# Kernel optimization log

Hardware: AMD Instinct MI355X
Metric: run time of the kernel (lower is better)

## Reference

```python
import jax, jax.numpy as jnp
import numpy as np

B, N, E, D, R = 32, 2048, 8192, 512, 8
V_SENSE = 25000
V_GLOBAL = 50000  # last_idx_globals - last_idx_senses


def setup_inputs() -> dict:
    key = jax.random.key(0)
    ks = jax.random.split(key, 12)
    x = jax.random.normal(ks[0], (B, N, D), dtype=jnp.float32)
    edge_index = jax.random.randint(ks[1], (B, 2, E), 0, N)
    edge_type = jax.random.randint(ks[2], (B, E), 0, R)
    s = 0.02
    basis = jax.random.normal(ks[3], (R, D, D), dtype=jnp.float32) * s   # num_bases = R
    comp = jax.random.normal(ks[4], (R, R), dtype=jnp.float32) * s      # [num_relations, num_bases]
    root = jax.random.normal(ks[5], (D, D), dtype=jnp.float32) * s
    bias_conv = jnp.zeros((D,), dtype=jnp.float32)
    w_global = jax.random.normal(ks[6], (V_GLOBAL, D), dtype=jnp.float32) * s
    b_global = jnp.zeros((V_GLOBAL,), dtype=jnp.float32)
    w_sense = jax.random.normal(ks[7], (V_SENSE, D), dtype=jnp.float32) * s
    b_sense = jnp.zeros((V_SENSE,), dtype=jnp.float32)
    return {"x": x, "edge_index": edge_index, "edge_type": edge_type,
            "basis": basis, "comp": comp, "root": root, "bias_conv": bias_conv,
            "w_global": w_global, "b_global": b_global,
            "w_sense": w_sense, "b_sense": b_sense}


def reference(x, edge_index, edge_type, basis, comp, root, bias_conv,
              w_global, b_global, w_sense, b_sense):
    # Basis decomposition: per-relation weight W_r = sum_b comp[r,b] * basis[b]
    W = jnp.einsum('rb,bio->rio', comp, basis)  # [R, D, D]

    def conv_one(xg, ei, et):
        # RGCNConv with mean aggregation per relation + root transform + bias
        src, dst = ei[0], ei[1]
        x_src = xg[src]                              # [E, D] gather
        out = xg @ root + bias_conv                  # [N, D]
        for r in range(R):                           # fixed small relation loop
            mask = (et == r).astype(xg.dtype)        # [E]
            msg = (x_src @ W[r]) * mask[:, None]     # [E, D]
            s = jax.ops.segment_sum(msg, dst, num_segments=N)              # [N, D]
            cnt = jax.ops.segment_sum(mask, dst, num_segments=N)           # [N]
            out = out + s / jnp.maximum(cnt, 1.0)[:, None]                 # mean aggr
        return out

    h = jax.vmap(conv_one)(x, edge_index, edge_type)  # [B, N, D]
    h = jax.nn.relu(h)
    h0 = h[:, 0]                                      # current node per sample [B, D]
    logits_global = h0 @ w_global.T + b_global        # [B, V_GLOBAL]
    logits_sense = h0 @ w_sense.T + b_sense           # [B, V_SENSE]
    return (jax.nn.log_softmax(logits_global, axis=-1),
            jax.nn.log_softmax(logits_sense, axis=-1))
```

## Files before the change

### kernel.cpp

```cpp
#include <hip/hip_runtime.h>
#include <hip/hip_bf16.h>

#define BATCH 32
#define NNODE 2048
#define NEDGE 8192
#define DIM   512
#define NREL  8
#define VG    50000
#define VS    25000
#define ZI    4608
#define NCH   36
#define GB3   391
#define SB3   196
#define PG    25
#define PS    13

typedef __attribute__((ext_vector_type(4))) float f32x4;
typedef __attribute__((ext_vector_type(8))) short s16x8;

__global__ __launch_bounds__(512) void k_conv(const float* __restrict__ x,
                                              const int* __restrict__ ei,
                                              const int* __restrict__ et,
                                              const float* __restrict__ comp,
                                              float* __restrict__ z) {
    int g = blockIdx.x;
    int t = threadIdx.x;
    int wv = t >> 6, lane = t & 63;
    __shared__ int elds[8 * 128];
    __shared__ int wcnt[8];
    const int* srcp = ei + (size_t)(g * 2 + 0) * NEDGE;
    const int* dstp = ei + (size_t)(g * 2 + 1) * NEDGE;

    int run = 0;
    for (int it = 0; it < 16; it++) {
        int e = wv * 1024 + it * 64 + lane;
        bool m = (dstp[e] == 0);
        unsigned long long mask = __ballot(m);
        int rank = __popcll(mask & ((1ull << lane) - 1ull));
        if (m && (run + rank) < 128) elds[wv * 128 + run + rank] = e;
        run += (int)__popcll(mask);
    }
    if (lane == 0) wcnt[wv] = (run > 128) ? 128 : run;
    __syncthreads();

    int d = t;
    float s0=0,s1=0,s2=0,s3=0,s4=0,s5=0,s6=0,s7=0;
    int   c0=0,c1=0,c2=0,c3=0,c4=0,c5=0,c6=0,c7=0;
    for (int w = 0; w < 8; w++) {
        int cw = wcnt[w];
        for (int i = 0; i < cw; i++) {
            int e = elds[w * 128 + i];
            int r = et[(size_t)g * NEDGE + e];
            int sn = srcp[e];
            float val = x[((size_t)g * NNODE + sn) * DIM + d];
            if (r == 0) { s0 += val; c0++; }
            if (r == 1) { s1 += val; c1++; }
            if (r == 2) { s2 += val; c2++; }
            if (r == 3) { s3 += val; c3++; }
            if (r == 4) { s4 += val; c4++; }
            if (r == 5) { s5 += val; c5++; }
            if (r == 6) { s6 += val; c6++; }
            if (r == 7) { s7 += val; c7++; }
        }
    }
    float sv[8] = {s0,s1,s2,s3,s4,s5,s6,s7};
    float inv[8];
    int   cv[8] = {c0,c1,c2,c3,c4,c5,c6,c7};
    #pragma unroll
    for (int r = 0; r < 8; r++) inv[r] = 1.0f / fmaxf((float)cv[r], 1.0f);

    z[(size_t)g * ZI + d] = x[((size_t)g * NNODE + 0) * DIM + d];
    #pragma unroll
    for (int b = 0; b < 8; b++) {
        float y = 0.f;
        #pragma unroll
        for (int r = 0; r < 8; r++) y += comp[r * 8 + b] * inv[r] * sv[r];
        z[(size_t)g * ZI + 512 + b * 512 + d] = y;
    }
}

__global__ __launch_bounds__(512) void k_gemm_part(const float* __restrict__ z,
                                                   const float* __restrict__ root,
                                                   const float* __restrict__ basis,
                                                   float* __restrict__ part2) {
    int bx = blockIdx.x;
    int dt = bx & 3;
    int cc = bx >> 2;
    int t = threadIdx.x;
    int dl = t & 127, gq = t >> 7;
    __shared__ float ztT[128][33];
    #pragma unroll
    for (int rep = 0; rep < 8; rep++) {
        int flat = rep * 512 + t;
        int g = flat >> 7, i = flat & 127;
        ztT[i][g] = z[(size_t)g * ZI + cc * 128 + i];
    }
    __syncthreads();
    const float* M = (cc < 4) ? (root + (size_t)(cc * 128) * 512)
                              : (basis + (size_t)((cc - 4) * 128) * 512);
    float acc[8] = {0,0,0,0,0,0,0,0};
    for (int i = 0; i < 128; i++) {
        float m = M[(size_t)i * 512 + dt * 128 + dl];
        #pragma unroll
        for (int j = 0; j < 8; j++) acc[j] += ztT[i][gq * 8 + j] * m;
    }
    #pragma unroll
    for (int j = 0; j < 8; j++) {
        int g = gq * 8 + j;
        part2[((size_t)cc * 32 + g) * 512 + dt * 128 + dl] = acc[j];
    }
}

__device__ __forceinline__ unsigned bf16rne(float f) {
    unsigned u = __float_as_uint(f);
    return (u + 0x7FFFu + ((u >> 16) & 1u)) >> 16;
}

__global__ __launch_bounds__(256) void k_h0(const float* __restrict__ part2,
                                            const float* __restrict__ bias_conv,
                                            unsigned* __restrict__ h0t) {
    int g = blockIdx.x;
    int p = threadIdx.x;
    int d0 = 2 * p;
    float v0 = bias_conv[d0], v1 = bias_conv[d0 + 1];
    for (int cc = 0; cc < NCH; cc++) {
        const float* pp = part2 + ((size_t)cc * 32 + g) * 512 + d0;
        v0 += pp[0];
        v1 += pp[1];
    }
    v0 = fmaxf(v0, 0.f);
    v1 = fmaxf(v1, 0.f);
    h0t[g * 256 + p] = bf16rne(v0) | (bf16rne(v1) << 16);
}

__device__ __forceinline__ void gload_lds16(const float* gsrc, float* ldst) {
    __builtin_amdgcn_global_load_lds(
        (const __attribute__((address_space(1))) void*)gsrc,
        (__attribute__((address_space(3))) void*)ldst,
        16, 0, 0);
}

__device__ __forceinline__ short f2bf(float f) {
    __hip_bfloat16 h = __float2bfloat16(f);
    return *reinterpret_cast<short*>(&h);
}

__global__ __launch_bounds__(256) void k_logits3(const unsigned* __restrict__ h0t,
                                                 const float* __restrict__ wg,
                                                 const float* __restrict__ bg,
                                                 const float* __restrict__ wsn,
                                                 const float* __restrict__ bsv,
                                                 float* __restrict__ out) {
    __shared__ __align__(16) unsigned char hlds[32768];
    __shared__ __align__(16) unsigned char wlds[2][16384];

    int t = threadIdx.x;
    int bx = blockIdx.x;
    int wv = t >> 6, l = t & 63;

    const float* w; const float* bias; float* ob; int V; int v0;
    if (bx < GB3) { w = wg;  bias = bg;  ob = out;                      V = VG; v0 = bx * 128; }
    else          { w = wsn; bias = bsv; ob = out + (size_t)BATCH * VG; V = VS; v0 = (bx - GB3) * 128; }
    int Vm1 = V - 1;

    #pragma unroll
    for (int rep = 0; rep < 8; rep++) {
        int idx = rep * 256 + t;
        int g = idx >> 6, q = idx & 63;
        uint4 val = *(const uint4*)&h0t[idx * 4];
        *(uint4*)&hlds[g * 1024 + ((q << 4) ^ ((g & 7) << 4))] = val;
    }

    #pragma unroll
    for (int i = 0; i < 4; i++) {
        int o = i * 256 + t;
        int row = o >> 3, g16 = o & 7;
        int vr = v0 + row; if (vr > Vm1) vr = Vm1;
        const float* src = w + (size_t)vr * 512
                         + ((((g16 << 4) ^ ((row & 3) << 5))) >> 2);
        gload_lds16(src, (float*)&wlds[0][o * 16]);
    }
    asm volatile("s_waitcnt vmcnt(0)" ::: "memory");
    __syncthreads();

    f32x4 acc[2][2];
    #pragma unroll
    for (int a = 0; a < 2; a++)
        #pragma unroll
        for (int b = 0; b < 2; b++) acc[a][b] = (f32x4){0.f, 0.f, 0.f, 0.f};

    int g32 = l >> 4;
    int gl  = l & 15;
    int cur = 0;

    for (int kc = 0; kc < 16; kc++) {
        if (kc < 15) {
            #pragma unroll
            for (int i = 0; i < 4; i++) {
                int o = i * 256 + t;
                int row = o >> 3, g16 = o & 7;
                int vr = v0 + row; if (vr > Vm1) vr = Vm1;
                const float* src = w + (size_t)vr * 512 + (kc + 1) * 32
                                 + ((((g16 << 4) ^ ((row & 3) << 5))) >> 2);
                gload_lds16(src, (float*)&wlds[cur ^ 1][o * 16]);
            }
        }

        int abase = (kc * 64 + g32 * 16) ^ ((gl & 7) << 4);
        s16x8 a0 = *(const s16x8*)&hlds[gl * 1024 + abase];
        s16x8 a1 = *(const s16x8*)&hlds[(gl + 16) * 1024 + abase];

        #pragma unroll
        for (int ntl = 0; ntl < 2; ntl++) {
            int rloc = (wv * 2 + ntl) * 16 + gl;
            int boff = rloc * 128 + ((g32 * 32) ^ ((rloc & 3) << 5));
            float4 blo = *(const float4*)&wlds[cur][boff];
            float4 bhi = *(const float4*)&wlds[cur][boff + 16];
            s16x8 bf;
            bf[0] = f2bf(blo.x); bf[1] = f2bf(blo.y);
            bf[2] = f2bf(blo.z); bf[3] = f2bf(blo.w);
            bf[4] = f2bf(bhi.x); bf[5] = f2bf(bhi.y);
            bf[6] = f2bf(bhi.z); bf[7] = f2bf(bhi.w);
            acc[ntl][0] = __builtin_amdgcn_mfma_f32_16x16x32_bf16(a0, bf, acc[ntl][0], 0, 0, 0);
            acc[ntl][1] = __builtin_amdgcn_mfma_f32_16x16x32_bf16(a1, bf, acc[ntl][1], 0, 0, 0);
        }

        asm volatile("s_waitcnt vmcnt(0)" ::: "memory");
        __syncthreads();
        cur ^= 1;
    }

    int lrowb = (l >> 4) * 4;
    #pragma unroll
    for (int ntl = 0; ntl < 2; ntl++) {
        int vv = v0 + (wv * 2 + ntl) * 16 + gl;
        if (vv < V) {
            float bia = bias[vv];
            #pragma unroll
            for (int mt = 0; mt < 2; mt++) {
                #pragma unroll
                for (int j = 0; j < 4; j++) {
                    int g = mt * 16 + lrowb + j;
                    ob[(size_t)g * V + vv] = acc[ntl][mt][j] + bia;
                }
            }
        }
    }
}

__global__ __launch_bounds__(256) void k_lse_part(const float* __restrict__ out,
                                                  float* __restrict__ part) {
    int bx = blockIdx.x;
    int V, ci, pidx;
    const float* row;
    if (bx < 32 * PG) {
        int g = bx / PG; ci = bx % PG; V = VG;
        row = out + (size_t)g * VG;
        pidx = g * PG + ci;
    } else {
        int b2 = bx - 32 * PG;
        int g = b2 / PS; ci = b2 % PS; V = VS;
        row = out + (size_t)BATCH * VG + (size_t)g * VS;
        pidx = 32 * PG + g * PS + ci;
    }
    int t = threadIdx.x;
    float p = 0.f;
    int base = ci * 2048 + t * 8;
    #pragma unroll
    for (int jj = 0; jj < 8; jj++) {
        int idx = base + jj;
        if (idx < V) p += expf(row[idx]);
    }
    #pragma unroll
    for (int s = 1; s < 64; s <<= 1) p += __shfl_xor(p, s);
    __shared__ float wsum[4];
    if ((t & 63) == 0) wsum[t >> 6] = p;
    __syncthreads();
    if (t == 0) part[pidx] = wsum[0] + wsum[1] + wsum[2] + wsum[3];
}

__global__ __launch_bounds__(64) void k_lse_final(const float* __restrict__ part,
                                                  float* __restrict__ lse) {
    int t = threadIdx.x;
    int head = t >> 5, g = t & 31;
    float s = 0.f;
    if (head == 0) { for (int c = 0; c < PG; c++) s += part[g * PG + c]; }
    else           { for (int c = 0; c < PS; c++) s += part[32 * PG + g * PS + c]; }
    lse[t] = logf(s);
}

__global__ __launch_bounds__(256) void k_sub(float* __restrict__ out,
                                             const float* __restrict__ lse) {
    unsigned i4 = blockIdx.x * 256u + threadIdx.x;
    if (i4 >= 600000u) return;
    unsigned idx = i4 * 4u;
    float l;
    if (idx < 1600000u) l = lse[idx / 50000u];
    else                l = lse[32u + (idx - 1600000u) / 25000u];
    float4 v = *(float4*)(out + idx);
    v.x -= l; v.y -= l; v.z -= l; v.w -= l;
    *(float4*)(out + idx) = v;
}

extern "C" void kernel_launch(void* const* d_in, const int* in_sizes, int n_in,
                              void* d_out, int out_size, void* d_ws, size_t ws_size,
                              hipStream_t stream) {
    const float* x        = (const float*)d_in[0];
    const int*   ei       = (const int*)  d_in[1];
    const int*   et       = (const int*)  d_in[2];
    const float* basis    = (const float*)d_in[3];
    const float* comp     = (const float*)d_in[4];
    const float* root     = (const float*)d_in[5];
    const float* biasc    = (const float*)d_in[6];
    const float* wg       = (const float*)d_in[7];
    const float* bg       = (const float*)d_in[8];
    const float* wsn      = (const float*)d_in[9];
    const float* bsv      = (const float*)d_in[10];
    float* out = (float*)d_out;

    float* z     = out;
    float* part2 = out + (size_t)BATCH * ZI;
    unsigned* h0t  = (unsigned*)d_ws;
    float*    plse = (float*)d_ws + 8192;
    float*    lse  = plse + 32 * PG + 32 * PS;

    k_conv     <<<BATCH, 512, 0, stream>>>(x, ei, et, comp, z);
    k_gemm_part<<<NCH * 4, 512, 0, stream>>>(z, root, basis, part2);
    k_h0       <<<BATCH, 256, 0, stream>>>(part2, biasc, h0t);
    k_logits3  <<<GB3 + SB3, 256, 0, stream>>>(h0t, wg, bg, wsn, bsv, out);
    k_lse_part <<<32 * PG + 32 * PS, 256, 0, stream>>>(out, plse);
    k_lse_final<<<1, 64, 0, stream>>>(plse, lse);
    k_sub      <<<2344, 256, 0, stream>>>(out, lse);
}
```

Baseline: 82.82 us.

## Triple-buffer weight tiles in logits GEMM with one barrier per k-step

The logits kernel moves from a double-buffered to a triple-buffered LDS pipeline for the fp32 vocabulary weight tiles. Two k-chunks are prefetched ahead, and it waits with a partial vmcnt so one chunk's loads stay in flight while the current chunk is computed. This leaves a single barrier per iteration instead of a full drain-and-sync. The h0 loads are issued into registers before the weight prefetch, the LDS swizzle is changed to an 8-way XOR, and launch bounds request 2 blocks per CU. The cost is 16KB more LDS per block, which may limit occupancy.

```diff
diff --git a/kernel.cpp b/kernel.cpp
--- a/kernel.cpp
+++ b/kernel.cpp
@@ -145,14 +145,14 @@
     return *reinterpret_cast<short*>(&h);
 }
 
-__global__ __launch_bounds__(256) void k_logits3(const unsigned* __restrict__ h0t,
-                                                 const float* __restrict__ wg,
-                                                 const float* __restrict__ bg,
-                                                 const float* __restrict__ wsn,
-                                                 const float* __restrict__ bsv,
-                                                 float* __restrict__ out) {
+__global__ __launch_bounds__(256, 2) void k_logits4(const unsigned* __restrict__ h0t,
+                                                    const float* __restrict__ wg,
+                                                    const float* __restrict__ bg,
+                                                    const float* __restrict__ wsn,
+                                                    const float* __restrict__ bsv,
+                                                    float* __restrict__ out) {
     __shared__ __align__(16) unsigned char hlds[32768];
-    __shared__ __align__(16) unsigned char wlds[2][16384];
+    __shared__ __align__(16) unsigned char wlds[3][16384];
 
     int t = threadIdx.x;
     int bx = blockIdx.x;
@@ -163,25 +163,31 @@
     else          { w = wsn; bias = bsv; ob = out + (size_t)BATCH * VG; V = VS; v0 = (bx - GB3) * 128; }
     int Vm1 = V - 1;
 
+    uint4 hv[8];
+    #pragma unroll
+    for (int rep = 0; rep < 8; rep++)
+        hv[rep] = *(const uint4*)&h0t[(rep * 256 + t) * 4];
+
+    #pragma unroll
+    for (int kc0 = 0; kc0 < 2; kc0++) {
+        #pragma unroll
+        for (int i = 0; i < 4; i++) {
+            int o = i * 256 + t;
+            int row = o >> 3, gq = o & 7;
+            int vr = v0 + row; if (vr > Vm1) vr = Vm1;
+            const float* src = w + (size_t)vr * 512 + kc0 * 32
+                             + ((gq ^ (row & 7)) << 2);
+            gload_lds16(src, (float*)&wlds[kc0][o * 16]);
+        }
+    }
+
     #pragma unroll
     for (int rep = 0; rep < 8; rep++) {
         int idx = rep * 256 + t;
         int g = idx >> 6, q = idx & 63;
-        uint4 val = *(const uint4*)&h0t[idx * 4];
-        *(uint4*)&hlds[g * 1024 + ((q << 4) ^ ((g & 7) << 4))] = val;
-    }
-
-    #pragma unroll
-    for (int i = 0; i < 4; i++) {
-        int o = i * 256 + t;
-        int row = o >> 3, g16 = o & 7;
-        int vr = v0 + row; if (vr > Vm1) vr = Vm1;
-        const float* src = w + (size_t)vr * 512
-                         + ((((g16 << 4) ^ ((row & 3) << 5))) >> 2);
-        gload_lds16(src, (float*)&wlds[0][o * 16]);
-    }
-    asm volatile("s_waitcnt vmcnt(0)" ::: "memory");
-    __syncthreads();
+        *(uint4*)&hlds[g * 1024 + ((q ^ (g & 7)) << 4)] = hv[rep];
+    }
+    asm volatile("s_waitcnt lgkmcnt(0)" ::: "memory");
 
     f32x4 acc[2][2];
     #pragma unroll
@@ -191,31 +197,24 @@
 
     int g32 = l >> 4;
     int gl  = l & 15;
-    int cur = 0;
+    int axor = (gl & 7) << 4;
 
     for (int kc = 0; kc < 16; kc++) {
-        if (kc < 15) {
-            #pragma unroll
-            for (int i = 0; i < 4; i++) {
-                int o = i * 256 + t;
-                int row = o >> 3, g16 = o & 7;
-                int vr = v0 + row; if (vr > Vm1) vr = Vm1;
-                const float* src = w + (size_t)vr * 512 + (kc + 1) * 32
-                                 + ((((g16 << 4) ^ ((row & 3) << 5))) >> 2);
-                gload_lds16(src, (float*)&wlds[cur ^ 1][o * 16]);
-            }
-        }
-
-        int abase = (kc * 64 + g32 * 16) ^ ((gl & 7) << 4);
-        s16x8 a0 = *(const s16x8*)&hlds[gl * 1024 + abase];
-        s16x8 a1 = *(const s16x8*)&hlds[(gl + 16) * 1024 + abase];
+        if (kc == 0 || kc == 15) { asm volatile("s_waitcnt vmcnt(0)" ::: "memory"); }
+        else                     { asm volatile("s_waitcnt vmcnt(4)" ::: "memory"); }
+        __builtin_amdgcn_s_barrier();
+
+        const unsigned char* wb = wlds[kc % 3];
+        int abase = kc * 64 + g32 * 16;
+        s16x8 a0 = *(const s16x8*)&hlds[gl * 1024 + (abase ^ axor)];
+        s16x8 a1 = *(const s16x8*)&hlds[(gl + 16) * 1024 + (abase ^ axor)];
 
         #pragma unroll
         for (int ntl = 0; ntl < 2; ntl++) {
             int rloc = (wv * 2 + ntl) * 16 + gl;
-            int boff = rloc * 128 + ((g32 * 32) ^ ((rloc & 3) << 5));
-            float4 blo = *(const float4*)&wlds[cur][boff];
-            float4 bhi = *(const float4*)&wlds[cur][boff + 16];
+            int s = rloc & 7;
+            float4 blo = *(const float4*)&wb[rloc * 128 + (((g32 * 2)     ^ s) << 4)];
+            float4 bhi = *(const float4*)&wb[rloc * 128 + (((g32 * 2 + 1) ^ s) << 4)];
             s16x8 bf;
             bf[0] = f2bf(blo.x); bf[1] = f2bf(blo.y);
             bf[2] = f2bf(blo.z); bf[3] = f2bf(blo.w);
@@ -225,9 +224,17 @@
             acc[ntl][1] = __builtin_amdgcn_mfma_f32_16x16x32_bf16(a1, bf, acc[ntl][1], 0, 0, 0);
         }
 
-        asm volatile("s_waitcnt vmcnt(0)" ::: "memory");
-        __syncthreads();
-        cur ^= 1;
+        if (kc + 2 < 16) {
+            #pragma unroll
+            for (int i = 0; i < 4; i++) {
+                int o = i * 256 + t;
+                int row = o >> 3, gq = o & 7;
+                int vr = v0 + row; if (vr > Vm1) vr = Vm1;
+                const float* src = w + (size_t)vr * 512 + (kc + 2) * 32
+                                 + ((gq ^ (row & 7)) << 2);
+                gload_lds16(src, (float*)&wlds[(kc + 2) % 3][o * 16]);
+            }
+        }
     }
 
     int lrowb = (l >> 4) * 4;
@@ -327,7 +334,7 @@
     k_conv     <<<BATCH, 512, 0, stream>>>(x, ei, et, comp, z);
     k_gemm_part<<<NCH * 4, 512, 0, stream>>>(z, root, basis, part2);
     k_h0       <<<BATCH, 256, 0, stream>>>(part2, biasc, h0t);
-    k_logits3  <<<GB3 + SB3, 256, 0, stream>>>(h0t, wg, bg, wsn, bsv, out);
+    k_logits4  <<<GB3 + SB3, 256, 0, stream>>>(h0t, wg, bg, wsn, bsv, out);
     k_lse_part <<<32 * PG + 32 * PS, 256, 0, stream>>>(out, plse);
     k_lse_final<<<1, 64, 0, stream>>>(plse, lse);
     k_sub      <<<2344, 256, 0, stream>>>(out, lse);
```

After: 78.33 us. 5.4% less time.
